# Optimization experiments

Measured on AMD Instinct MI355X. Metric: run time of the kernel, lower is better.

Reference implementation:

```python
import jax, jax.numpy as jnp
import numpy as np

B, N, NKV = 2, 2048, 2048
E = 4096
H = 16
HD = E // H          # 256 head_dim
LQ = E // 8          # 512 q latent
LKV = E // 16        # 256 kv latent


def setup_inputs() -> dict:
    key = jax.random.key(0)
    ks = jax.random.split(key, 6)
    Q = jax.random.normal(ks[0], (B, N, E), dtype=jnp.float32)
    K = jax.random.normal(ks[1], (B, NKV, E), dtype=jnp.float32)
    # Linear weights stored as (in, out); scaled ~1/sqrt(fan_in) like torch default init
    Wq_d = jax.random.normal(ks[2], (E, LQ), dtype=jnp.float32) / np.sqrt(E)
    W_qk = jax.random.normal(ks[3], (LQ, H * LKV), dtype=jnp.float32) / np.sqrt(LQ)
    Wkv_d = jax.random.normal(ks[4], (E, LKV), dtype=jnp.float32) / np.sqrt(E)
    Wv_u = jax.random.normal(ks[5], (LKV, H * HD), dtype=jnp.float32) / np.sqrt(LKV)
    return {"Q": Q, "K": K, "Wq_d": Wq_d, "W_qk": W_qk, "Wkv_d": Wkv_d, "Wv_u": Wv_u}


def reference(Q, K, Wq_d, W_qk, Wkv_d, Wv_u):
    b, n, _ = Q.shape
    nkv = K.shape[1]
    C_q = Q @ Wq_d                                   # [B,N,Lq]
    C_kv = K @ Wkv_d                                 # [B,Nkv,Lkv]
    CqWqk = (C_q @ W_qk).reshape(b, n, H, LKV)       # [B,N,H,Lkv]
    # scores contract over the kv latent dim (absorbed-weight MLA)
    scores = jnp.einsum('bnhl,bkl->bhnk', CqWqk, C_kv) / jnp.sqrt(
        jnp.asarray(LKV, dtype=Q.dtype))             # [B,H,N,Nkv]
    attn = jax.nn.softmax(scores, axis=-1)
    V_up = (C_kv @ Wv_u).reshape(b, nkv, H, HD)      # [B,Nkv,H,hd]
    out = jnp.einsum('bhnk,bkhd->bnhd', attn, V_up)  # [B,N,H,hd]
    return out.reshape(b, n, H * HD)                 # [B,N,E]
```

## Files before the change

kernel.cpp:

```cpp
#include <hip/hip_runtime.h>


#define B_ 2
#define N_ 2048
#define H_ 16
#define HD_ 256
#define LKV_ 256

typedef __attribute__((ext_vector_type(8))) short bf8;
typedef __attribute__((ext_vector_type(4))) float f4;
typedef __attribute__((ext_vector_type(4))) unsigned short us4v;
typedef unsigned short u16;

__device__ __forceinline__ u16 f2b(float f) {
  union { float f; unsigned u; } v; v.f = f;
  unsigned r = (v.u + 0x7FFFu + ((v.u >> 16) & 1u)) >> 16;
  return (u16)r;
}

__device__ __forceinline__ void load_lds16(const void* g, void* l) {
  __builtin_amdgcn_global_load_lds(
      (const __attribute__((address_space(1))) unsigned int*)(unsigned long long)(uintptr_t)g,
      (__attribute__((address_space(3))) unsigned int*)(unsigned int)(uintptr_t)l,
      16, 0, 0);
}

__global__ __launch_bounds__(256) void cvt_bf16_2(const float* __restrict__ a,
                                                  u16* __restrict__ da,
                                                  const float* __restrict__ b,
                                                  u16* __restrict__ db, int n4)
{
  int i = blockIdx.x * 256 + threadIdx.x;
  const float* s; u16* d;
  if (i < n4) { s = a; d = da; } else { s = b; d = db; i -= n4; }
  float4 v = *(const float4*)(s + (size_t)i * 4);
  us4v o = {f2b(v.x), f2b(v.y), f2b(v.z), f2b(v.w)};
  *(us4v*)(d + (size_t)i * 4) = o;
}

__global__ __launch_bounds__(256) void cvt_transpose(const float* __restrict__ src,
                                                     u16* __restrict__ dst, int R, int C)
{
  __shared__ float tile[32][33];
  const int t = threadIdx.x;
  const int tr = t & 31, tc = t >> 5;
  const int r0 = blockIdx.x * 32, c0 = blockIdx.y * 32;
#pragma unroll
  for (int i = 0; i < 4; ++i)
    tile[tc + i * 8][tr] = src[(size_t)(r0 + tc + i * 8) * C + c0 + tr];
  __syncthreads();
#pragma unroll
  for (int i = 0; i < 4; ++i)
    dst[(size_t)(c0 + tc + i * 8) * R + r0 + tr] = f2b(tile[tr][tc + i * 8]);
}

__global__ __launch_bounds__(256) void gemm_bt(
    const u16* __restrict__ A,
    const u16* __restrict__ Bt,
    u16* __restrict__ C,
    int M, int N, int K)
{
  __shared__ u16 As[128 * 32];
  __shared__ u16 Bs[128 * 32];

  const int t = threadIdx.x;
  const int w = t >> 6, lane = t & 63;
  const int quad = lane >> 4, l16 = lane & 15;
  const int n0 = blockIdx.x * 128, m0 = blockIdx.y * 128;
  const int wm = (w >> 1) * 64, wn = (w & 1) * 64;

  f4 acc[4][4];
#pragma unroll
  for (int mi = 0; mi < 4; ++mi)
#pragma unroll
    for (int ni = 0; ni < 4; ++ni) acc[mi][ni] = (f4){0.f, 0.f, 0.f, 0.f};

  const u16* Ap = A + (size_t)m0 * K;
  const u16* Bp = Bt + (size_t)n0 * K;
  const int srow = t >> 2, spos = (t & 3) * 8;

  for (int k0 = 0; k0 < K; k0 += 32) {
    __syncthreads();
    load_lds16(Ap + (size_t)srow * K + k0 + spos,        &As[(size_t)t * 8]);
    load_lds16(Ap + (size_t)(srow + 64) * K + k0 + spos, &As[(size_t)(256 + t) * 8]);
    load_lds16(Bp + (size_t)srow * K + k0 + spos,        &Bs[(size_t)t * 8]);
    load_lds16(Bp + (size_t)(srow + 64) * K + k0 + spos, &Bs[(size_t)(256 + t) * 8]);
    __syncthreads();

    bf8 af[4], bfr[4];
#pragma unroll
    for (int mi = 0; mi < 4; ++mi)
      af[mi] = *(const bf8*)(&As[(wm + mi * 16 + l16) * 32 + quad * 8]);
#pragma unroll
    for (int ni = 0; ni < 4; ++ni)
      bfr[ni] = *(const bf8*)(&Bs[(wn + ni * 16 + l16) * 32 + quad * 8]);
#pragma unroll
    for (int mi = 0; mi < 4; ++mi)
#pragma unroll
      for (int ni = 0; ni < 4; ++ni)
        acc[mi][ni] = __builtin_amdgcn_mfma_f32_16x16x32_bf16(af[mi], bfr[ni], acc[mi][ni], 0, 0, 0);
  }

  u16* Cp = C + (size_t)m0 * N + n0;
#pragma unroll
  for (int mi = 0; mi < 4; ++mi)
#pragma unroll
    for (int r = 0; r < 4; ++r) {
      int m = wm + mi * 16 + quad * 4 + r;
#pragma unroll
      for (int ni = 0; ni < 4; ++ni)
        Cp[(size_t)m * N + wn + ni * 16 + l16] = f2b(acc[mi][ni][r]);
    }
}

__global__ __launch_bounds__(256) void gemm_qkv(
    const u16* __restrict__ Aq, const u16* __restrict__ Bq, u16* __restrict__ Cq,
    const u16* __restrict__ Ak, const u16* __restrict__ Bk, u16* __restrict__ Ck)
{
  const int K = 4096;
  __shared__ u16 As[128 * 32];
  __shared__ u16 Bs[64 * 32];

  const u16* A; const u16* Bt; u16* C; int N, n0;
  if (blockIdx.x < 8) { A = Aq; Bt = Bq; C = Cq; N = 512; n0 = blockIdx.x * 64; }
  else               { A = Ak; Bt = Bk; C = Ck; N = 256; n0 = (blockIdx.x - 8) * 64; }

  const int t = threadIdx.x;
  const int w = t >> 6, lane = t & 63;
  const int quad = lane >> 4, l16 = lane & 15;
  const int m0 = blockIdx.y * 128;
  const int wm = (w >> 1) * 64, wn = (w & 1) * 32;

  f4 acc[4][2];
#pragma unroll
  for (int mi = 0; mi < 4; ++mi)
#pragma unroll
    for (int ni = 0; ni < 2; ++ni) acc[mi][ni] = (f4){0.f, 0.f, 0.f, 0.f};

  const u16* Ap = A + (size_t)m0 * K;
  const u16* Bp = Bt + (size_t)n0 * K;
  const int srow = t >> 2, spos = (t & 3) * 8;

  for (int k0 = 0; k0 < K; k0 += 32) {
    __syncthreads();
    load_lds16(Ap + (size_t)srow * K + k0 + spos,        &As[(size_t)t * 8]);
    load_lds16(Ap + (size_t)(srow + 64) * K + k0 + spos, &As[(size_t)(256 + t) * 8]);
    load_lds16(Bp + (size_t)srow * K + k0 + spos,        &Bs[(size_t)t * 8]);
    __syncthreads();

    bf8 af[4], bfr[2];
#pragma unroll
    for (int mi = 0; mi < 4; ++mi)
      af[mi] = *(const bf8*)(&As[(wm + mi * 16 + l16) * 32 + quad * 8]);
#pragma unroll
    for (int ni = 0; ni < 2; ++ni)
      bfr[ni] = *(const bf8*)(&Bs[(wn + ni * 16 + l16) * 32 + quad * 8]);
#pragma unroll
    for (int mi = 0; mi < 4; ++mi)
#pragma unroll
      for (int ni = 0; ni < 2; ++ni)
        acc[mi][ni] = __builtin_amdgcn_mfma_f32_16x16x32_bf16(af[mi], bfr[ni], acc[mi][ni], 0, 0, 0);
  }

  u16* Cp = C + (size_t)m0 * N + n0;
#pragma unroll
  for (int mi = 0; mi < 4; ++mi)
#pragma unroll
    for (int r = 0; r < 4; ++r) {
      int m = wm + mi * 16 + quad * 4 + r;
#pragma unroll
      for (int ni = 0; ni < 2; ++ni)
        Cp[(size_t)m * N + wn + ni * 16 + l16] = f2b(acc[mi][ni][r]);
    }
}

__global__ __launch_bounds__(256) void transpose_v(const u16* __restrict__ vupB,
                                                   u16* __restrict__ vupT)
{
  __shared__ u16 tile[64][78];
  const int t = threadIdx.x;
  const int key0 = blockIdx.x * 64, d0 = blockIdx.y * 64;
  const int bh = blockIdx.z, b = bh >> 4, h = bh & 15;

#pragma unroll
  for (int i = 0; i < 2; ++i) {
    int c = t + 256 * i;
    int key = c >> 3, d8 = c & 7;
    bf8 v = *(const bf8*)(vupB + ((size_t)(b * N_ + key0 + key) * (H_ * HD_)) + h * HD_ + d0 + d8 * 8);
    *(bf8*)(&tile[key][d8 * 8]) = v;
  }
  __syncthreads();
#pragma unroll
  for (int i = 0; i < 2; ++i) {
    int c = t + 256 * i;
    int d = c >> 3, k8 = c & 7;
    bf8 v;
#pragma unroll
    for (int j = 0; j < 8; ++j) v[j] = (short)tile[k8 * 8 + j][d];
    *(bf8*)(vupT + ((size_t)bh * HD_ + d0 + d) * (size_t)N_ + key0 + k8 * 8) = v;
  }
}

__global__ __launch_bounds__(256, 2) void flash_mfma(
    const u16* __restrict__ q2b,
    const u16* __restrict__ ckvb,
    const u16* __restrict__ vupT,
    float* __restrict__ out)
{
  __shared__ u16 KtL[2][32 * 256];
  __shared__ u16 VtL[2][256 * 32];
  __shared__ u16 PtL[128 * 40];

  const int t = threadIdx.x;
  const int w = t >> 6, lane = t & 63;
  const int quad = lane >> 4, l16 = lane & 15;
  const int n0 = blockIdx.x * 128;
  const int bh = blockIdx.y, b = bh >> 4, h = bh & 15;

  bf8 qf[2][8];
  {
    const u16* qbase = q2b + (size_t)(b * N_ + n0 + w * 32 + l16) * (H_ * LKV_) + h * LKV_ + quad * 8;
#pragma unroll
    for (int mi = 0; mi < 2; ++mi)
#pragma unroll
      for (int ks = 0; ks < 8; ++ks)
        qf[mi][ks] = *(const bf8*)(qbase + (size_t)(mi * 16) * (H_ * LKV_) + ks * 32);
  }

  f4 o[2][16];
#pragma unroll
  for (int mi = 0; mi < 2; ++mi)
#pragma unroll
    for (int dt = 0; dt < 16; ++dt) o[mi][dt] = (f4){0.f, 0.f, 0.f, 0.f};
  float ms[2][4], ls[2][4];
#pragma unroll
  for (int mi = 0; mi < 2; ++mi)
#pragma unroll
    for (int r = 0; r < 4; ++r) { ms[mi][r] = -1e30f; ls[mi][r] = 0.f; }

  const u16* kgb = ckvb + (size_t)b * N_ * LKV_;
  const u16* vgb = vupT + (size_t)bh * HD_ * N_;

  int krow[4], kscol[4], vd[4], vscol[4];
#pragma unroll
  for (int i = 0; i < 4; ++i) {
    int c = i * 256 + t;
    krow[i]  = c >> 5;
    kscol[i] = (c & 31) ^ (krow[i] & 7);
    vd[i]    = c >> 2;
    vscol[i] = (c & 3) ^ (vd[i] & 3);
  }

  auto stage = [&](int buf, int k0) {
#pragma unroll
    for (int i = 0; i < 4; ++i)
      load_lds16(kgb + (size_t)(k0 + krow[i]) * LKV_ + kscol[i] * 8,
                 &KtL[buf][(i * 256 + t) * 8]);
#pragma unroll
    for (int i = 0; i < 4; ++i)
      load_lds16(vgb + (size_t)vd[i] * N_ + k0 + vscol[i] * 8,
                 &VtL[buf][(i * 256 + t) * 8]);
  };

  stage(0, 0);
  int cur = 0;
  const int kswz = l16 & 7;
  const int vq8  = (quad ^ (l16 & 3)) * 8;

  for (int k0 = 0; k0 < N_; k0 += 32) {
    __syncthreads();
    if (k0 + 32 < N_) stage(cur ^ 1, k0 + 32);

    f4 sf[2][2];
    sf[0][0] = (f4){0,0,0,0}; sf[0][1] = (f4){0,0,0,0};
    sf[1][0] = (f4){0,0,0,0}; sf[1][1] = (f4){0,0,0,0};
    __builtin_amdgcn_s_setprio(1);
#pragma unroll
    for (int nt = 0; nt < 2; ++nt) {
      const u16* kr = &KtL[cur][(nt * 16 + l16) * 256];
#pragma unroll
      for (int ks = 0; ks < 8; ++ks) {
        bf8 kf = *(const bf8*)(kr + (((quad + ks * 4) ^ kswz) << 3));
        sf[0][nt] = __builtin_amdgcn_mfma_f32_16x16x32_bf16(qf[0][ks], kf, sf[0][nt], 0, 0, 0);
        sf[1][nt] = __builtin_amdgcn_mfma_f32_16x16x32_bf16(qf[1][ks], kf, sf[1][nt], 0, 0, 0);
      }
    }
    __builtin_amdgcn_s_setprio(0);

#pragma unroll
    for (int mi = 0; mi < 2; ++mi) {
      float al[4];
#pragma unroll
      for (int r = 0; r < 4; ++r) {
        float a0 = sf[mi][0][r] * 0.0625f;
        float a1 = sf[mi][1][r] * 0.0625f;
        float mx = fmaxf(a0, a1);
#pragma unroll
        for (int off = 1; off < 16; off <<= 1) mx = fmaxf(mx, __shfl_xor(mx, off, 16));
        float mn = fmaxf(ms[mi][r], mx);
        float p0 = __expf(a0 - mn), p1 = __expf(a1 - mn);
        float sum = p0 + p1;
#pragma unroll
        for (int off = 1; off < 16; off <<= 1) sum += __shfl_xor(sum, off, 16);
        al[r] = __expf(ms[mi][r] - mn);
        ls[mi][r] = ls[mi][r] * al[r] + sum;
        ms[mi][r] = mn;
        int q = w * 32 + mi * 16 + quad * 4 + r;
        PtL[q * 40 + l16]      = f2b(p0);
        PtL[q * 40 + 16 + l16] = f2b(p1);
      }
#pragma unroll
      for (int dt = 0; dt < 16; ++dt) {
        o[mi][dt][0] *= al[0]; o[mi][dt][1] *= al[1];
        o[mi][dt][2] *= al[2]; o[mi][dt][3] *= al[3];
      }
    }

    bf8 pf0 = *(const bf8*)(&PtL[(w * 32 + l16) * 40 + quad * 8]);
    bf8 pf1 = *(const bf8*)(&PtL[(w * 32 + 16 + l16) * 40 + quad * 8]);

    __builtin_amdgcn_s_setprio(1);
#pragma unroll
    for (int dt = 0; dt < 16; ++dt) {
      bf8 vf = *(const bf8*)(&VtL[cur][(dt * 16 + l16) * 32 + vq8]);
      o[0][dt] = __builtin_amdgcn_mfma_f32_16x16x32_bf16(pf0, vf, o[0][dt], 0, 0, 0);
      o[1][dt] = __builtin_amdgcn_mfma_f32_16x16x32_bf16(pf1, vf, o[1][dt], 0, 0, 0);
    }
    __builtin_amdgcn_s_setprio(0);

    cur ^= 1;
  }

#pragma unroll
  for (int mi = 0; mi < 2; ++mi)
#pragma unroll
    for (int r = 0; r < 4; ++r) {
      float iv = 1.f / ls[mi][r];
      float* dst = out + (size_t)(b * N_ + n0 + w * 32 + mi * 16 + quad * 4 + r) * (H_ * HD_)
                   + h * HD_ + l16;
#pragma unroll
      for (int dt = 0; dt < 16; ++dt) dst[dt * 16] = o[mi][dt][r] * iv;
    }
}

extern "C" void kernel_launch(void* const* d_in, const int* in_sizes, int n_in,
                              void* d_out, int out_size, void* d_ws, size_t ws_size,
                              hipStream_t stream) {
  const float* Q     = (const float*)d_in[0];
  const float* Kin   = (const float*)d_in[1];
  const float* Wq_d  = (const float*)d_in[2];
  const float* W_qk  = (const float*)d_in[3];
  const float* Wkv_d = (const float*)d_in[4];
  const float* Wv_u  = (const float*)d_in[5];
  float* out = (float*)d_out;

  char* ws = (char*)d_ws;
  u16* qbf   = (u16*)(ws);
  u16* vupT  = qbf;
  u16* kbf   = (u16*)(ws + 33554432);
  u16* vupB  = kbf;
  u16* q2b   = (u16*)(ws + 67108864);
  u16* cqb   = (u16*)(ws + 100663296);
  u16* ckvb  = (u16*)(ws + 104857600);
  u16* wqdT  = (u16*)(ws + 106954752);
  u16* wqkT  = (u16*)(ws + 111149056);
  u16* wkvdT = (u16*)(ws + 115343360);
  u16* wvuT  = (u16*)(ws + 117440512);

  cvt_bf16_2<<<dim3(32768), 256, 0, stream>>>(Q, qbf, Kin, kbf, 4194304);
  cvt_transpose<<<dim3(128, 16), 256, 0, stream>>>(Wq_d,  wqdT,  4096, 512);
  cvt_transpose<<<dim3(16, 128), 256, 0, stream>>>(W_qk,  wqkT,  512, 4096);
  cvt_transpose<<<dim3(128, 8),  256, 0, stream>>>(Wkv_d, wkvdT, 4096, 256);
  cvt_transpose<<<dim3(8, 128),  256, 0, stream>>>(Wv_u,  wvuT,  256, 4096);

  gemm_qkv<<<dim3(12, 32), 256, 0, stream>>>(qbf, wqdT, cqb, kbf, wkvdT, ckvb);
  gemm_bt<<<dim3(32, 32), 256, 0, stream>>>(cqb, wqkT, q2b, 4096, 4096, 512);
  gemm_bt<<<dim3(32, 32), 256, 0, stream>>>(ckvb, wvuT, vupB, 4096, 4096, 256);
  transpose_v<<<dim3(32, 4, 32), 256, 0, stream>>>(vupB, vupT);
  flash_mfma<<<dim3(16, 32), 256, 0, stream>>>(q2b, ckvb, vupT, out);
}
```

Measured before the change: 687.1 us.

## Shrink flash attention tile to 64 queries, single-buffer LDS, XCD-aware block mapping

The flash kernel now handles 64 query rows per block (16 per wave) instead of 128, which halves per-thread accumulators and Q fragments. Occupancy rises to 4 blocks per CU and the grid grows to 1024 blocks. The K/V LDS tiles drop from double to single buffering, with a second barrier per iteration in place of prefetch overlap. Blocks are remapped so each XCD handles a contiguous set of batch-heads, improving L2 reuse of K/V. The trade-off is that K/V tiles are reloaded twice as often per query and load latency is no longer hidden by prefetch, so it relies on occupancy to cover that latency.

```diff
diff --git a/kernel.cpp b/kernel.cpp
--- a/kernel.cpp
+++ b/kernel.cpp
@@ -201,146 +201,122 @@
   }
 }
 
-__global__ __launch_bounds__(256, 2) void flash_mfma(
+__global__ __launch_bounds__(256, 4) void flash_mfma(
     const u16* __restrict__ q2b,
     const u16* __restrict__ ckvb,
     const u16* __restrict__ vupT,
     float* __restrict__ out)
 {
-  __shared__ u16 KtL[2][32 * 256];
-  __shared__ u16 VtL[2][256 * 32];
-  __shared__ u16 PtL[128 * 40];
+  __shared__ u16 KtL[32 * 256];
+  __shared__ u16 VtL[256 * 32];
+  __shared__ u16 PtL[64 * 36];
 
   const int t = threadIdx.x;
   const int w = t >> 6, lane = t & 63;
   const int quad = lane >> 4, l16 = lane & 15;
-  const int n0 = blockIdx.x * 128;
-  const int bh = blockIdx.y, b = bh >> 4, h = bh & 15;
-
-  bf8 qf[2][8];
+
+  const int wg = blockIdx.x;
+  const int xcd = wg & 7, idx = wg >> 3;
+  const int bh = xcd * 4 + (idx >> 5);
+  const int n0 = (idx & 31) * 64;
+  const int b = bh >> 4, h = bh & 15;
+
+  bf8 qf[8];
   {
-    const u16* qbase = q2b + (size_t)(b * N_ + n0 + w * 32 + l16) * (H_ * LKV_) + h * LKV_ + quad * 8;
-#pragma unroll
-    for (int mi = 0; mi < 2; ++mi)
-#pragma unroll
-      for (int ks = 0; ks < 8; ++ks)
-        qf[mi][ks] = *(const bf8*)(qbase + (size_t)(mi * 16) * (H_ * LKV_) + ks * 32);
-  }
-
-  f4 o[2][16];
-#pragma unroll
-  for (int mi = 0; mi < 2; ++mi)
-#pragma unroll
-    for (int dt = 0; dt < 16; ++dt) o[mi][dt] = (f4){0.f, 0.f, 0.f, 0.f};
-  float ms[2][4], ls[2][4];
-#pragma unroll
-  for (int mi = 0; mi < 2; ++mi)
-#pragma unroll
-    for (int r = 0; r < 4; ++r) { ms[mi][r] = -1e30f; ls[mi][r] = 0.f; }
+    const u16* qbase = q2b + (size_t)(b * N_ + n0 + w * 16 + l16) * (H_ * LKV_) + h * LKV_ + quad * 8;
+#pragma unroll
+    for (int ks = 0; ks < 8; ++ks)
+      qf[ks] = *(const bf8*)(qbase + ks * 32);
+  }
+
+  f4 o[16];
+#pragma unroll
+  for (int dt = 0; dt < 16; ++dt) o[dt] = (f4){0.f, 0.f, 0.f, 0.f};
+  float ms[4], ls[4];
+#pragma unroll
+  for (int r = 0; r < 4; ++r) { ms[r] = -1e30f; ls[r] = 0.f; }
 
   const u16* kgb = ckvb + (size_t)b * N_ * LKV_;
   const u16* vgb = vupT + (size_t)bh * HD_ * N_;
 
-  int krow[4], kscol[4], vd[4], vscol[4];
-#pragma unroll
-  for (int i = 0; i < 4; ++i) {
-    int c = i * 256 + t;
-    krow[i]  = c >> 5;
-    kscol[i] = (c & 31) ^ (krow[i] & 7);
-    vd[i]    = c >> 2;
-    vscol[i] = (c & 3) ^ (vd[i] & 3);
-  }
-
-  auto stage = [&](int buf, int k0) {
-#pragma unroll
-    for (int i = 0; i < 4; ++i)
-      load_lds16(kgb + (size_t)(k0 + krow[i]) * LKV_ + kscol[i] * 8,
-                 &KtL[buf][(i * 256 + t) * 8]);
-#pragma unroll
-    for (int i = 0; i < 4; ++i)
-      load_lds16(vgb + (size_t)vd[i] * N_ + k0 + vscol[i] * 8,
-                 &VtL[buf][(i * 256 + t) * 8]);
-  };
-
-  stage(0, 0);
-  int cur = 0;
   const int kswz = l16 & 7;
   const int vq8  = (quad ^ (l16 & 3)) * 8;
 
   for (int k0 = 0; k0 < N_; k0 += 32) {
     __syncthreads();
-    if (k0 + 32 < N_) stage(cur ^ 1, k0 + 32);
-
-    f4 sf[2][2];
-    sf[0][0] = (f4){0,0,0,0}; sf[0][1] = (f4){0,0,0,0};
-    sf[1][0] = (f4){0,0,0,0}; sf[1][1] = (f4){0,0,0,0};
+#pragma unroll
+    for (int i = 0; i < 4; ++i) {
+      int c = i * 256 + t;
+      int kr = c >> 5, kc = (c & 31) ^ (kr & 7);
+      load_lds16(kgb + (size_t)(k0 + kr) * LKV_ + kc * 8, &KtL[c * 8]);
+    }
+#pragma unroll
+    for (int i = 0; i < 4; ++i) {
+      int c = i * 256 + t;
+      int vr = c >> 2, vc = (c & 3) ^ (vr & 3);
+      load_lds16(vgb + (size_t)vr * N_ + k0 + vc * 8, &VtL[c * 8]);
+    }
+    __syncthreads();
+
+    f4 sf[2];
+    sf[0] = (f4){0,0,0,0}; sf[1] = (f4){0,0,0,0};
     __builtin_amdgcn_s_setprio(1);
 #pragma unroll
     for (int nt = 0; nt < 2; ++nt) {
-      const u16* kr = &KtL[cur][(nt * 16 + l16) * 256];
+      const u16* kr = &KtL[(nt * 16 + l16) * 256];
 #pragma unroll
       for (int ks = 0; ks < 8; ++ks) {
         bf8 kf = *(const bf8*)(kr + (((quad + ks * 4) ^ kswz) << 3));
-        sf[0][nt] = __builtin_amdgcn_mfma_f32_16x16x32_bf16(qf[0][ks], kf, sf[0][nt], 0, 0, 0);
-        sf[1][nt] = __builtin_amdgcn_mfma_f32_16x16x32_bf16(qf[1][ks], kf, sf[1][nt], 0, 0, 0);
+        sf[nt] = __builtin_amdgcn_mfma_f32_16x16x32_bf16(qf[ks], kf, sf[nt], 0, 0, 0);
       }
     }
     __builtin_amdgcn_s_setprio(0);
 
-#pragma unroll
-    for (int mi = 0; mi < 2; ++mi) {
-      float al[4];
-#pragma unroll
-      for (int r = 0; r < 4; ++r) {
-        float a0 = sf[mi][0][r] * 0.0625f;
-        float a1 = sf[mi][1][r] * 0.0625f;
-        float mx = fmaxf(a0, a1);
-#pragma unroll
-        for (int off = 1; off < 16; off <<= 1) mx = fmaxf(mx, __shfl_xor(mx, off, 16));
-        float mn = fmaxf(ms[mi][r], mx);
-        float p0 = __expf(a0 - mn), p1 = __expf(a1 - mn);
-        float sum = p0 + p1;
-#pragma unroll
-        for (int off = 1; off < 16; off <<= 1) sum += __shfl_xor(sum, off, 16);
-        al[r] = __expf(ms[mi][r] - mn);
-        ls[mi][r] = ls[mi][r] * al[r] + sum;
-        ms[mi][r] = mn;
-        int q = w * 32 + mi * 16 + quad * 4 + r;
-        PtL[q * 40 + l16]      = f2b(p0);
-        PtL[q * 40 + 16 + l16] = f2b(p1);
-      }
-#pragma unroll
-      for (int dt = 0; dt < 16; ++dt) {
-        o[mi][dt][0] *= al[0]; o[mi][dt][1] *= al[1];
-        o[mi][dt][2] *= al[2]; o[mi][dt][3] *= al[3];
-      }
-    }
-
-    bf8 pf0 = *(const bf8*)(&PtL[(w * 32 + l16) * 40 + quad * 8]);
-    bf8 pf1 = *(const bf8*)(&PtL[(w * 32 + 16 + l16) * 40 + quad * 8]);
+    float al[4];
+#pragma unroll
+    for (int r = 0; r < 4; ++r) {
+      float a0 = sf[0][r] * 0.0625f;
+      float a1 = sf[1][r] * 0.0625f;
+      float mx = fmaxf(a0, a1);
+#pragma unroll
+      for (int off = 1; off < 16; off <<= 1) mx = fmaxf(mx, __shfl_xor(mx, off, 16));
+      float mn = fmaxf(ms[r], mx);
+      float p0 = __expf(a0 - mn), p1 = __expf(a1 - mn);
+      float sum = p0 + p1;
+#pragma unroll
+      for (int off = 1; off < 16; off <<= 1) sum += __shfl_xor(sum, off, 16);
+      al[r] = __expf(ms[r] - mn);
+      ls[r] = ls[r] * al[r] + sum;
+      ms[r] = mn;
+      int q = w * 16 + quad * 4 + r;
+      PtL[q * 36 + l16]      = f2b(p0);
+      PtL[q * 36 + 16 + l16] = f2b(p1);
+    }
+#pragma unroll
+    for (int dt = 0; dt < 16; ++dt) {
+      o[dt][0] *= al[0]; o[dt][1] *= al[1];
+      o[dt][2] *= al[2]; o[dt][3] *= al[3];
+    }
+
+    bf8 pf = *(const bf8*)(&PtL[(w * 16 + l16) * 36 + quad * 8]);
 
     __builtin_amdgcn_s_setprio(1);
 #pragma unroll
     for (int dt = 0; dt < 16; ++dt) {
-      bf8 vf = *(const bf8*)(&VtL[cur][(dt * 16 + l16) * 32 + vq8]);
-      o[0][dt] = __builtin_amdgcn_mfma_f32_16x16x32_bf16(pf0, vf, o[0][dt], 0, 0, 0);
-      o[1][dt] = __builtin_amdgcn_mfma_f32_16x16x32_bf16(pf1, vf, o[1][dt], 0, 0, 0);
+      bf8 vf = *(const bf8*)(&VtL[(dt * 16 + l16) * 32 + vq8]);
+      o[dt] = __builtin_amdgcn_mfma_f32_16x16x32_bf16(pf, vf, o[dt], 0, 0, 0);
     }
     __builtin_amdgcn_s_setprio(0);
-
-    cur ^= 1;
-  }
-
-#pragma unroll
-  for (int mi = 0; mi < 2; ++mi)
-#pragma unroll
-    for (int r = 0; r < 4; ++r) {
-      float iv = 1.f / ls[mi][r];
-      float* dst = out + (size_t)(b * N_ + n0 + w * 32 + mi * 16 + quad * 4 + r) * (H_ * HD_)
-                   + h * HD_ + l16;
-#pragma unroll
-      for (int dt = 0; dt < 16; ++dt) dst[dt * 16] = o[mi][dt][r] * iv;
-    }
+  }
+
+#pragma unroll
+  for (int r = 0; r < 4; ++r) {
+    float iv = 1.f / ls[r];
+    float* dst = out + (size_t)(b * N_ + n0 + w * 16 + quad * 4 + r) * (H_ * HD_)
+                 + h * HD_ + l16;
+#pragma unroll
+    for (int dt = 0; dt < 16; ++dt) dst[dt * 16] = o[dt][r] * iv;
+  }
 }
 
 extern "C" void kernel_launch(void* const* d_in, const int* in_sizes, int n_in,
@@ -377,5 +353,5 @@
   gemm_bt<<<dim3(32, 32), 256, 0, stream>>>(cqb, wqkT, q2b, 4096, 4096, 512);
   gemm_bt<<<dim3(32, 32), 256, 0, stream>>>(ckvb, wvuT, vupB, 4096, 4096, 256);
   transpose_v<<<dim3(32, 4, 32), 256, 0, stream>>>(vupB, vupT);
-  flash_mfma<<<dim3(16, 32), 256, 0, stream>>>(q2b, ckvb, vupT, out);
-}
+  flash_mfma<<<dim3(1024), 256, 0, stream>>>(q2b, ckvb, vupT, out);
+}
```

Result: slower. 1.106 ms (+61.0%).
